# Optimization experiments

Hardware: AMD Instinct MI355X
Metric: run time of the kernel (lower is better)

Reference implementation:

```python
import jax, jax.numpy as jnp
import numpy as np

B, S, D, H, DFF = 2, 2048, 1024, 16, 4096
DK = D // H
EPS = 1e-6


def setup_inputs() -> dict:
    key = jax.random.key(0)
    ks = jax.random.split(key, 16)
    sd = 0.02
    inp = {
        "x": jax.random.normal(ks[0], (B, S, D), jnp.float32),
        "mask": jnp.zeros((1, 1, S, S), jnp.float32),
        "wq": jax.random.normal(ks[1], (D, D), jnp.float32) * sd,
        "bq": jnp.zeros((D,), jnp.float32),
        "wk": jax.random.normal(ks[2], (D, D), jnp.float32) * sd,
        "bk": jnp.zeros((D,), jnp.float32),
        "wv": jax.random.normal(ks[3], (D, D), jnp.float32) * sd,
        "bv": jnp.zeros((D,), jnp.float32),
        "wo": jax.random.normal(ks[4], (D, D), jnp.float32) * sd,
        "bo": jnp.zeros((D,), jnp.float32),
        "w1": jax.random.normal(ks[5], (DFF, D), jnp.float32) * sd,
        "b1": jnp.zeros((DFF,), jnp.float32),
        "w2": jax.random.normal(ks[6], (D, DFF), jnp.float32) * sd,
        "b2": jnp.zeros((D,), jnp.float32),
        "alpha": jnp.ones((1,), jnp.float32),
        "gamma": jnp.zeros((1,), jnp.float32),
    }
    return inp


def _layer_norm(x, alpha, gamma):
    mean = jnp.mean(x, axis=-1, keepdims=True)
    var = jnp.mean((x - mean) ** 2, axis=-1, keepdims=True)
    return alpha * (x - mean) / jnp.sqrt(var + EPS) + gamma


def reference(x, mask, wq, bq, wk, bk, wv, bv, wo, bo, w1, b1, w2, b2, alpha, gamma):
    # --- multi-head attention (hand-rolled, full NxN scores) ---
    q = (x @ wq.T + bq).reshape(B, S, H, DK).transpose(0, 2, 1, 3)  # [B,H,S,DK]
    k = (x @ wk.T + bk).reshape(B, S, H, DK).transpose(0, 2, 1, 3)
    v = (x @ wv.T + bv).reshape(B, S, H, DK).transpose(0, 2, 1, 3)
    scores = jnp.einsum('bhqd,bhkd->bhqk', q, k) / np.sqrt(DK)  # [B,H,S,S]
    scores = scores + mask
    attn = jax.nn.softmax(scores, axis=-1)
    ctx = jnp.einsum('bhqk,bhkd->bhqd', attn, v)  # [B,H,S,DK]
    ctx = ctx.transpose(0, 2, 1, 3).reshape(B, S, D)
    attn_out = ctx @ wo.T + bo
    # residual + LayerNorm (dropout is identity in eval)
    out1 = _layer_norm(x + attn_out, alpha, gamma)
    # --- position-wise feed-forward ---
    ffn = jax.nn.relu(out1 @ w1.T + b1) @ w2.T + b2
    out2 = _layer_norm(out1 + ffn, alpha, gamma)
    return out2
```

## Files before the change

### kernel.cpp

```cpp
#include <hip/hip_runtime.h>


typedef float  f32x4   __attribute__((ext_vector_type(4)));
typedef float  f32x16  __attribute__((ext_vector_type(16)));
typedef __bf16 bf16x8  __attribute__((ext_vector_type(8)));
typedef __bf16 bf16x4  __attribute__((ext_vector_type(4)));

#define DEVI static __device__ __forceinline__

DEVI f32x4 mfma16(bf16x8 a, bf16x8 b, f32x4 c) {
    return __builtin_amdgcn_mfma_f32_16x16x32_bf16(a, b, c, 0, 0, 0);
}
DEVI f32x16 mfma32(bf16x8 a, bf16x8 b, f32x16 c) {
    return __builtin_amdgcn_mfma_f32_32x32x16_bf16(a, b, c, 0, 0, 0);
}

DEVI void gll16(const void* g, void* l) {
    __builtin_amdgcn_global_load_lds(
        (__attribute__((address_space(1))) void*)g,
        (__attribute__((address_space(3))) void*)l, 16, 0, 0);
}

DEVI __bf16 f2bf(float f) { return (__bf16)f; }

DEVI unsigned cvtpk_bf16(float a, float b) {
    unsigned d;
    asm("v_cvt_pk_bf16_f32 %0, %1, %2" : "=v"(d) : "v"(a), "v"(b));
    return d;
}
DEVI void permswap(unsigned& a, unsigned& b) {
    asm("v_permlane32_swap_b32 %0, %1" : "+v"(a), "+v"(b));
}
DEVI void permswapf(float& a, float& b) {
    asm("v_permlane32_swap_b32 %0, %1" : "+v"(a), "+v"(b));
}

__global__ void init_flag_kernel(int* f) { *f = 0; }

__global__ void mask_scan_kernel(const float* __restrict__ m, int* __restrict__ flag) {
    size_t i = (size_t)blockIdx.x * 256 + threadIdx.x;
    const float4* p = (const float4*)m;
    float4 a = p[i * 2], b = p[i * 2 + 1];
    bool nz = a.x != 0.f || a.y != 0.f || a.z != 0.f || a.w != 0.f ||
              b.x != 0.f || b.y != 0.f || b.z != 0.f || b.w != 0.f;
    if (__ballot(nz)) { if ((threadIdx.x & 63) == 0) atomicOr(flag, 1); }
}

__global__ void cast_bf16_kernel(const float* __restrict__ in, __bf16* __restrict__ out, int n8) {
    int i = blockIdx.x * 256 + threadIdx.x;
    if (i >= n8) return;
    const float4* p = (const float4*)in + (size_t)i * 2;
    float4 a = p[0], b = p[1];
    bf16x8 o = { (__bf16)a.x, (__bf16)a.y, (__bf16)a.z, (__bf16)a.w,
                 (__bf16)b.x, (__bf16)b.y, (__bf16)b.z, (__bf16)b.w };
    *(bf16x8*)(out + (size_t)i * 8) = o;
}

__global__ __launch_bounds__(256) void cast_weights_kernel(
    const float* __restrict__ wq, const float* __restrict__ wk,
    const float* __restrict__ wv, const float* __restrict__ wo,
    const float* __restrict__ w1, const float* __restrict__ w2,
    __bf16* __restrict__ wqb, __bf16* __restrict__ wkb,
    __bf16* __restrict__ wvb, __bf16* __restrict__ wob,
    __bf16* __restrict__ w1b, __bf16* __restrict__ w2b) {
    int i = blockIdx.x * 256 + threadIdx.x;
    const float* src; __bf16* dst; int off;
    if      (i <  131072) { src = wq; dst = wqb; off = i; }
    else if (i <  262144) { src = wk; dst = wkb; off = i -  131072; }
    else if (i <  393216) { src = wv; dst = wvb; off = i -  262144; }
    else if (i <  524288) { src = wo; dst = wob; off = i -  393216; }
    else if (i < 1048576) { src = w1; dst = w1b; off = i -  524288; }
    else                  { src = w2; dst = w2b; off = i - 1048576; }
    const float4* p = (const float4*)src + (size_t)off * 2;
    float4 a = p[0], b = p[1];
    bf16x8 o = { (__bf16)a.x, (__bf16)a.y, (__bf16)a.z, (__bf16)a.w,
                 (__bf16)b.x, (__bf16)b.y, (__bf16)b.z, (__bf16)b.w };
    *(bf16x8*)(dst + (size_t)off * 8) = o;
}

__global__ __launch_bounds__(256) void add_ln_kernel(
    const float* __restrict__ X, const float* __restrict__ Y,
    const float* __restrict__ alphap, const float* __restrict__ gammap,
    float* __restrict__ outF, __bf16* __restrict__ outB) {
    const int tid = threadIdx.x, lane = tid & 63, wid = tid >> 6;
    const size_t base = (size_t)blockIdx.x * 1024 + tid * 4;
    float4 xv = *(const float4*)&X[base];
    float4 yv = *(const float4*)&Y[base];
    float vx = xv.x + yv.x, vy = xv.y + yv.y, vz = xv.z + yv.z, vw = xv.w + yv.w;
    float s = vx + vy + vz + vw;
    #pragma unroll
    for (int o = 32; o; o >>= 1) s += __shfl_xor(s, o);
    __shared__ float red[4];
    if (lane == 0) red[wid] = s;
    __syncthreads();
    float mean = (red[0] + red[1] + red[2] + red[3]) * (1.0f / 1024.0f);
    float dx = vx - mean, dy = vy - mean, dz = vz - mean, dw = vw - mean;
    float s2 = dx * dx + dy * dy + dz * dz + dw * dw;
    #pragma unroll
    for (int o = 32; o; o >>= 1) s2 += __shfl_xor(s2, o);
    __syncthreads();
    if (lane == 0) red[wid] = s2;
    __syncthreads();
    float var = (red[0] + red[1] + red[2] + red[3]) * (1.0f / 1024.0f);
    float rstd = rsqrtf(var + 1e-6f);
    float a = alphap[0], g = gammap[0];
    float4 o4 = { a * dx * rstd + g, a * dy * rstd + g, a * dz * rstd + g, a * dw * rstd + g };
    *(float4*)&outF[base] = o4;
    if (outB) {
        bf16x4 ob = { f2bf(o4.x), f2bf(o4.y), f2bf(o4.z), f2bf(o4.w) };
        *(bf16x4*)&outB[base] = ob;
    }
}

template <int N, int K, int BN, int MODE>
__global__ __launch_bounds__(256, 3) void gemm_bt_kernel(
    const __bf16* __restrict__ A, const __bf16* __restrict__ W,
    const float* __restrict__ bias, void* __restrict__ outp) {
    constexpr int WN = BN / 2;
    constexpr int NI = WN / 16;
    __shared__ __bf16 lsA[128 * 64];
    __shared__ __bf16 lsB[BN * 64];
    const int tid = threadIdx.x, wid = tid >> 6, lane = tid & 63;
    const int wr = wid >> 1, wc = wid & 1, l15 = lane & 15, hi = lane >> 4;
    const int m0 = blockIdx.y * 128, n0 = blockIdx.x * BN;
    f32x4 acc[4][NI] = {};
    for (int kt = 0; kt < K / 64; ++kt) {
        #pragma unroll
        for (int i = 0; i < 4; ++i) {
            int row = wid * 32 + i * 8 + (lane >> 3);
            gll16(A + (size_t)(m0 + row) * K + kt * 64 + ((lane & 7) ^ (row & 7)) * 8,
                  &lsA[(wid * 32 + i * 8) * 64]);
        }
        #pragma unroll
        for (int i = 0; i < BN / 32; ++i) {
            int row = wid * (BN / 4) + i * 8 + (lane >> 3);
            gll16(W + (size_t)(n0 + row) * K + kt * 64 + ((lane & 7) ^ (row & 7)) * 8,
                  &lsB[(wid * (BN / 4) + i * 8) * 64]);
        }
        __syncthreads();
        #pragma unroll
        for (int s = 0; s < 2; ++s) {
            bf16x8 af[4], bfv[NI];
            #pragma unroll
            for (int mi = 0; mi < 4; ++mi) {
                int row = wr * 64 + mi * 16 + l15;
                af[mi] = *(const bf16x8*)&lsA[row * 64 + (((s * 4 + hi) ^ (row & 7)) * 8)];
            }
            #pragma unroll
            for (int ni = 0; ni < NI; ++ni) {
                int row = wc * WN + ni * 16 + l15;
                bfv[ni] = *(const bf16x8*)&lsB[row * 64 + (((s * 4 + hi) ^ (row & 7)) * 8)];
            }
            #pragma unroll
            for (int mi = 0; mi < 4; ++mi)
                #pragma unroll
                for (int ni = 0; ni < NI; ++ni)
                    acc[mi][ni] = mfma16(af[mi], bfv[ni], acc[mi][ni]);
        }
        __syncthreads();
    }
    #pragma unroll
    for (int ni = 0; ni < NI; ++ni) {
        int col = n0 + wc * WN + ni * 16 + l15;
        float bv = bias[col];
        #pragma unroll
        for (int mi = 0; mi < 4; ++mi) {
            int rowb = m0 + wr * 64 + mi * 16 + hi * 4;
            #pragma unroll
            for (int r = 0; r < 4; ++r) {
                float v = acc[mi][ni][r] + bv;
                if (MODE == 0) {
                    ((float*)outp)[(size_t)(rowb + r) * N + col] = v;
                } else {
                    v = fmaxf(v, 0.f);
                    ((__bf16*)outp)[(size_t)(rowb + r) * N + col] = f2bf(v);
                }
            }
        }
    }
}

template <int N, int K>
__global__ __launch_bounds__(512, 1) void gemm_pipe_kernel(
    const __bf16* __restrict__ A, const __bf16* __restrict__ W,
    const float* __restrict__ bias, __bf16* __restrict__ outp) {
    constexpr int NT = K / 64;
    __shared__ __bf16 lsA[3][256 * 64];
    __shared__ __bf16 lsB[3][128 * 64];
    const int tid = threadIdx.x, wid = tid >> 6, lane = tid & 63;
    const int wr = wid >> 1, wc = wid & 1, l15 = lane & 15, hi = lane >> 4;
    const int bid = blockIdx.x;
    const int tile = (bid & 7) * 64 + (bid >> 3);
    const int m0 = (tile >> 5) * 256, n0 = (tile & 31) * 128;

    f32x4 acc[4][4] = {};

    const int rl = wid * 8 + (lane >> 3);
    const int c8 = lane & 7;

    auto stageT = [&](int slot, int kt) {
        #pragma unroll
        for (int j = 0; j < 4; ++j) {
            int r = j * 64 + rl;
            gll16(A + (size_t)(m0 + r) * K + kt * 64 + (c8 ^ (r & 7)) * 8,
                  &lsA[slot][(j * 64 + wid * 8) * 64]);
        }
        #pragma unroll
        for (int j = 0; j < 2; ++j) {
            int r = j * 64 + rl;
            gll16(W + (size_t)(n0 + r) * K + kt * 64 + (c8 ^ (r & 7)) * 8,
                  &lsB[slot][(j * 64 + wid * 8) * 64]);
        }
    };

    stageT(0, 0);
    stageT(1, 1);
    asm volatile("s_waitcnt vmcnt(6)\ns_barrier" ::: "memory");

    for (int t = 0; t < NT; ++t) {
        if (t + 2 < NT) stageT((t + 2) % 3, t + 2);
        const __bf16* As = &lsA[t % 3][0];
        const __bf16* Bs = &lsB[t % 3][0];
        __builtin_amdgcn_s_setprio(1);
        #pragma unroll
        for (int s = 0; s < 2; ++s) {
            bf16x8 af[4], bfv[4];
            #pragma unroll
            for (int mi = 0; mi < 4; ++mi) {
                int row = wr * 64 + mi * 16 + l15;
                af[mi] = *(const bf16x8*)&As[row * 64 + (((s * 4 + hi) ^ (row & 7)) * 8)];
            }
            #pragma unroll
            for (int ni = 0; ni < 4; ++ni) {
                int row = wc * 64 + ni * 16 + l15;
                bfv[ni] = *(const bf16x8*)&Bs[row * 64 + (((s * 4 + hi) ^ (row & 7)) * 8)];
            }
            #pragma unroll
            for (int mi = 0; mi < 4; ++mi)
                #pragma unroll
                for (int ni = 0; ni < 4; ++ni)
                    acc[mi][ni] = mfma16(af[mi], bfv[ni], acc[mi][ni]);
        }
        __builtin_amdgcn_s_setprio(0);
        if (t < NT - 2) {
            asm volatile("s_waitcnt vmcnt(6)\ns_barrier" ::: "memory");
        } else if (t == NT - 2) {
            asm volatile("s_waitcnt vmcnt(0)\ns_barrier" ::: "memory");
        }
    }

    #pragma unroll
    for (int ni = 0; ni < 4; ++ni) {
        int col = n0 + wc * 64 + ni * 16 + l15;
        float bv = bias[col];
        #pragma unroll
        for (int mi = 0; mi < 4; ++mi) {
            int rowb = m0 + wr * 64 + mi * 16 + hi * 4;
            #pragma unroll
            for (int r = 0; r < 4; ++r) {
                float v = fmaxf(acc[mi][ni][r] + bv, 0.f);
                outp[(size_t)(rowb + r) * N + col] = f2bf(v);
            }
        }
    }
}

__global__ __launch_bounds__(256, 3) void gemm_qkv_kernel(
    const __bf16* __restrict__ A,
    const __bf16* __restrict__ wq, const __bf16* __restrict__ wk, const __bf16* __restrict__ wv,
    const float* __restrict__ bq, const float* __restrict__ bk, const float* __restrict__ bv,
    __bf16* __restrict__ q, __bf16* __restrict__ k, __bf16* __restrict__ vt) {
    constexpr int K = 1024;
    const int z = blockIdx.z;
    const __bf16* W = (z == 0) ? wq : (z == 1) ? wk : wv;
    const float* bias = (z == 0) ? bq : (z == 1) ? bk : bv;
    __shared__ __bf16 lsA[128 * 64];
    __shared__ __bf16 lsB[128 * 64];
    const int tid = threadIdx.x, wid = tid >> 6, lane = tid & 63;
    const int wr = wid >> 1, wc = wid & 1, l15 = lane & 15, hi = lane >> 4;
    const int m0 = blockIdx.y * 128, n0 = blockIdx.x * 128;
    f32x4 acc[4][4] = {};
    for (int kt = 0; kt < K / 64; ++kt) {
        #pragma unroll
        for (int i = 0; i < 4; ++i) {
            int row = wid * 32 + i * 8 + (lane >> 3);
            gll16(A + (size_t)(m0 + row) * K + kt * 64 + ((lane & 7) ^ (row & 7)) * 8,
                  &lsA[(wid * 32 + i * 8) * 64]);
            gll16(W + (size_t)(n0 + row) * K + kt * 64 + ((lane & 7) ^ (row & 7)) * 8,
                  &lsB[(wid * 32 + i * 8) * 64]);
        }
        __syncthreads();
        #pragma unroll
        for (int s = 0; s < 2; ++s) {
            bf16x8 af[4], bfv[4];
            #pragma unroll
            for (int mi = 0; mi < 4; ++mi) {
                int row = wr * 64 + mi * 16 + l15;
                af[mi] = *(const bf16x8*)&lsA[row * 64 + (((s * 4 + hi) ^ (row & 7)) * 8)];
            }
            #pragma unroll
            for (int ni = 0; ni < 4; ++ni) {
                int row = wc * 64 + ni * 16 + l15;
                bfv[ni] = *(const bf16x8*)&lsB[row * 64 + (((s * 4 + hi) ^ (row & 7)) * 8)];
            }
            #pragma unroll
            for (int mi = 0; mi < 4; ++mi)
                #pragma unroll
                for (int ni = 0; ni < 4; ++ni)
                    acc[mi][ni] = mfma16(af[mi], bfv[ni], acc[mi][ni]);
        }
        __syncthreads();
    }
    const float scale = (z == 0) ? 0.125f * 1.4426950408889634f : 1.0f;
    #pragma unroll
    for (int ni = 0; ni < 4; ++ni) {
        int col = n0 + wc * 64 + ni * 16 + l15;
        int h = col >> 6, dk = col & 63;
        float bvv = bias[col];
        #pragma unroll
        for (int mi = 0; mi < 4; ++mi) {
            int rowb = m0 + wr * 64 + mi * 16 + hi * 4;
            int b_ = rowb >> 11, sb = rowb & 2047;
            if (z < 2) {
                __bf16* dst = (z == 0) ? q : k;
                #pragma unroll
                for (int r = 0; r < 4; ++r)
                    dst[((size_t)(b_ * 16 + h) * 2048 + sb + r) * 64 + dk] =
                        f2bf((acc[mi][ni][r] + bvv) * scale);
            } else {
                bf16x4 o = { f2bf(acc[mi][ni][0] + bvv), f2bf(acc[mi][ni][1] + bvv),
                             f2bf(acc[mi][ni][2] + bvv), f2bf(acc[mi][ni][3] + bvv) };
                *(bf16x4*)&vt[((size_t)(b_ * 16 + h) * 64 + dk) * 2048 + sb] = o;
            }
        }
    }
}

__global__ __launch_bounds__(256, 2) void flash_attn_kernel(
    const __bf16* __restrict__ Q, const __bf16* __restrict__ Kx,
    const __bf16* __restrict__ VT, const float* __restrict__ mask,
    const int* __restrict__ mflag, __bf16* __restrict__ ctx) {
    __shared__ __bf16 Kl[2][64 * 64];
    __shared__ __bf16 Vl[2][64 * 64];
    const int lane = threadIdx.x & 63, wid = threadIdx.x >> 6;
    const int l31 = lane & 31, h = lane >> 5;
    const int id = blockIdx.x;
    const int xcd = id & 7, rest = id >> 3;
    const int qt = rest & 15;
    const int bh = (rest >> 4) * 8 + xcd;
    const int q0 = qt * 128 + wid * 32;

    bf16x8 qf[4];
    const size_t qrow = (size_t)bh * 2048 + q0 + l31;
    #pragma unroll
    for (int st = 0; st < 4; ++st)
        qf[st] = *(const bf16x8*)&Q[qrow * 64 + st * 16 + h * 8];

    const __bf16* kbase = Kx + (size_t)bh * 2048 * 64;
    const __bf16* vbase = VT + (size_t)bh * 64 * 2048;

    f32x16 c0 = {}, c1 = {};
    f32x16 lv = {};
    const bool useMask = (*mflag != 0);

    const int r0 = wid * 16;
    const int rA = r0 + (lane >> 3);
    const int rB = rA + 8;
    const int cA = (lane & 7) ^ (rA & 7);
    const int cB = (lane & 7) ^ (rB & 7);

    auto stage = [&](int b, int t) {
        gll16(kbase + (size_t)(t * 64 + rA) * 64 + cA * 8, &Kl[b][r0 * 64]);
        gll16(kbase + (size_t)(t * 64 + rB) * 64 + cB * 8, &Kl[b][(r0 + 8) * 64]);
        gll16(vbase + (size_t)rA * 2048 + t * 64 + cA * 8, &Vl[b][r0 * 64]);
        gll16(vbase + (size_t)rB * 2048 + t * 64 + cB * 8, &Vl[b][(r0 + 8) * 64]);
    };

    stage(0, 0);
    __syncthreads();
    int cur = 0;

    for (int t = 0; t < 32; ++t) {
        const int tn = (t + 1 < 32) ? t + 1 : t;
        stage(cur ^ 1, tn);
        #pragma unroll
        for (int s = 0; s < 2; ++s) {
            const int krow = s * 32 + l31;
            f32x16 sc = {};
            __builtin_amdgcn_s_setprio(1);
            #pragma unroll
            for (int st = 0; st < 4; ++st) {
                bf16x8 kf = *(const bf16x8*)&Kl[cur][krow * 64 + (((st * 2 + h) ^ (krow & 7)) * 8)];
                sc = mfma32(kf, qf[st], sc);
            }
            __builtin_amdgcn_s_setprio(0);
            if (useMask) {
                #pragma unroll
                for (int r = 0; r < 16; ++r) {
                    int kv = t * 64 + s * 32 + (r & 3) + 8 * (r >> 2) + 4 * h;
                    sc[r] += mask[(size_t)(q0 + l31) * 2048 + kv] * 1.4426950408889634f;
                }
            }
            #pragma unroll
            for (int r = 0; r < 16; ++r) sc[r] = exp2f(sc[r] - 40.0f);
            lv += sc;
            unsigned w0 = cvtpk_bf16(sc[0], sc[1]),   w2 = cvtpk_bf16(sc[4], sc[5]);
            unsigned w1 = cvtpk_bf16(sc[2], sc[3]),   w3 = cvtpk_bf16(sc[6], sc[7]);
            permswap(w0, w2); permswap(w1, w3);
            unsigned w4 = cvtpk_bf16(sc[8], sc[9]),   w6 = cvtpk_bf16(sc[12], sc[13]);
            unsigned w5 = cvtpk_bf16(sc[10], sc[11]), w7 = cvtpk_bf16(sc[14], sc[15]);
            permswap(w4, w6); permswap(w5, w7);
            uint4 u0 = { w0, w1, w2, w3 }, u1 = { w4, w5, w6, w7 };
            bf16x8 pb0, pb1;
            __builtin_memcpy(&pb0, &u0, 16);
            __builtin_memcpy(&pb1, &u1, 16);
            const int vr0 = l31, vr1 = 32 + l31;
            bf16x8 v00 = *(const bf16x8*)&Vl[cur][vr0 * 64 + (((s * 4 + 0 + h) ^ (vr0 & 7)) * 8)];
            bf16x8 v01 = *(const bf16x8*)&Vl[cur][vr0 * 64 + (((s * 4 + 2 + h) ^ (vr0 & 7)) * 8)];
            bf16x8 v10 = *(const bf16x8*)&Vl[cur][vr1 * 64 + (((s * 4 + 0 + h) ^ (vr1 & 7)) * 8)];
            bf16x8 v11 = *(const bf16x8*)&Vl[cur][vr1 * 64 + (((s * 4 + 2 + h) ^ (vr1 & 7)) * 8)];
            __builtin_amdgcn_s_setprio(1);
            c0 = mfma32(v00, pb0, c0);
            c0 = mfma32(v01, pb1, c0);
            c1 = mfma32(v10, pb0, c1);
            c1 = mfma32(v11, pb1, c1);
            __builtin_amdgcn_s_setprio(0);
        }
        __syncthreads();
        cur ^= 1;
    }

    float y8[8], y4[4];
    #pragma unroll
    for (int r = 0; r < 8; ++r) y8[r] = lv[2 * r] + lv[2 * r + 1];
    #pragma unroll
    for (int r = 0; r < 4; ++r) y4[r] = y8[2 * r] + y8[2 * r + 1];
    float ls = (y4[0] + y4[1]) + (y4[2] + y4[3]);
    float la = ls, lb = ls;
    permswapf(la, lb);
    const float rinv = 1.0f / (la + lb);

    const int b_ = bh >> 4, h_ = bh & 15;
    const size_t obase = ((size_t)b_ * 2048 + q0 + l31) * 1024 + (size_t)h_ * 64;
    #pragma unroll
    for (int g = 0; g < 4; ++g) {
        bf16x4 o0 = { f2bf(c0[4 * g + 0] * rinv), f2bf(c0[4 * g + 1] * rinv),
                      f2bf(c0[4 * g + 2] * rinv), f2bf(c0[4 * g + 3] * rinv) };
        *(bf16x4*)&ctx[obase + g * 8 + h * 4] = o0;
        bf16x4 o1 = { f2bf(c1[4 * g + 0] * rinv), f2bf(c1[4 * g + 1] * rinv),
                      f2bf(c1[4 * g + 2] * rinv), f2bf(c1[4 * g + 3] * rinv) };
        *(bf16x4*)&ctx[obase + 32 + g * 8 + h * 4] = o1;
    }
}

extern "C" void kernel_launch(void* const* d_in, const int* in_sizes, int n_in,
                              void* d_out, int out_size, void* d_ws, size_t ws_size,
                              hipStream_t stream) {
    const float* x     = (const float*)d_in[0];
    const float* mask  = (const float*)d_in[1];
    const float* wq    = (const float*)d_in[2];
    const float* bq    = (const float*)d_in[3];
    const float* wk    = (const float*)d_in[4];
    const float* bk    = (const float*)d_in[5];
    const float* wv    = (const float*)d_in[6];
    const float* bv    = (const float*)d_in[7];
    const float* wo    = (const float*)d_in[8];
    const float* bo    = (const float*)d_in[9];
    const float* w1    = (const float*)d_in[10];
    const float* b1    = (const float*)d_in[11];
    const float* w2    = (const float*)d_in[12];
    const float* b2    = (const float*)d_in[13];
    const float* alpha = (const float*)d_in[14];
    const float* gamma = (const float*)d_in[15];

    char* ws = (char*)d_ws;
    const size_t MB = 1u << 20;
    __bf16* xb    = (__bf16*)(ws + 0 * MB);
    __bf16* qb    = (__bf16*)(ws + 8 * MB);
    __bf16* kb    = (__bf16*)(ws + 16 * MB);
    __bf16* vtb   = (__bf16*)(ws + 24 * MB);
    __bf16* ctxb  = (__bf16*)(ws + 32 * MB);
    __bf16* wqb   = (__bf16*)(ws + 40 * MB);
    __bf16* wkb   = (__bf16*)(ws + 42 * MB);
    __bf16* wvb   = (__bf16*)(ws + 44 * MB);
    __bf16* wob   = (__bf16*)(ws + 46 * MB);
    __bf16* w1b   = (__bf16*)(ws + 48 * MB);
    __bf16* w2b   = (__bf16*)(ws + 56 * MB);
    float*  attn  = (float*)(ws + 64 * MB);
    float*  out1  = (float*)(ws + 80 * MB);
    __bf16* out1b = (__bf16*)(ws + 96 * MB);
    __bf16* hid   = (__bf16*)(ws + 104 * MB);
    int*    mflag = (int*)(ws + 136 * MB);
    if (ws_size < 136 * MB + 64) return;

    init_flag_kernel<<<1, 1, 0, stream>>>(mflag);
    mask_scan_kernel<<<2048, 256, 0, stream>>>(mask, mflag);

    cast_bf16_kernel<<<2048, 256, 0, stream>>>(x, xb, 524288);
    cast_weights_kernel<<<6144, 256, 0, stream>>>(wq, wk, wv, wo, w1, w2,
                                                  wqb, wkb, wvb, wob, w1b, w2b);

    gemm_qkv_kernel<<<dim3(8, 32, 3), 256, 0, stream>>>(xb, wqb, wkb, wvb, bq, bk, bv,
                                                        qb, kb, vtb);
    flash_attn_kernel<<<dim3(512), 256, 0, stream>>>(qb, kb, vtb, mask, mflag, ctxb);
    gemm_bt_kernel<1024, 1024, 64, 0><<<dim3(16, 32), 256, 0, stream>>>(ctxb, wob, bo, attn);
    add_ln_kernel<<<4096, 256, 0, stream>>>(x, attn, alpha, gamma, out1, out1b);
    gemm_pipe_kernel<4096, 1024><<<dim3(512), 512, 0, stream>>>(out1b, w1b, b1, hid);
    gemm_bt_kernel<1024, 4096, 64, 0><<<dim3(16, 32), 256, 0, stream>>>(hid, w2b, b2, attn);
    add_ln_kernel<<<4096, 256, 0, stream>>>(out1, attn, alpha, gamma, (float*)d_out, nullptr);
}
```

Before: 273.3 us.

## Merge cast kernels, store intermediates in bf16, replace FFN1 GEMM with 128x128 tiles

Merges the x and weight bf16 casts into a single launch. Stores the attention-projection and FFN-down outputs as bf16 instead of fp32, and drops the fp32 out1 copy, so the second LayerNorm reads the bf16 residual. This cuts intermediate memory traffic at some precision cost in the residual path. It also replaces the 512-thread 256x128 pipelined FFN1 GEMM with a 256-thread 128x128 tile kernel using K=32 triple buffering, running 3 blocks per CU and more blocks overall.

```diff
diff --git a/kernel.cpp b/kernel.cpp
--- a/kernel.cpp
+++ b/kernel.cpp
@@ -46,31 +46,24 @@
     if (__ballot(nz)) { if ((threadIdx.x & 63) == 0) atomicOr(flag, 1); }
 }
 
-__global__ void cast_bf16_kernel(const float* __restrict__ in, __bf16* __restrict__ out, int n8) {
-    int i = blockIdx.x * 256 + threadIdx.x;
-    if (i >= n8) return;
-    const float4* p = (const float4*)in + (size_t)i * 2;
-    float4 a = p[0], b = p[1];
-    bf16x8 o = { (__bf16)a.x, (__bf16)a.y, (__bf16)a.z, (__bf16)a.w,
-                 (__bf16)b.x, (__bf16)b.y, (__bf16)b.z, (__bf16)b.w };
-    *(bf16x8*)(out + (size_t)i * 8) = o;
-}
-
-__global__ __launch_bounds__(256) void cast_weights_kernel(
+__global__ __launch_bounds__(256) void cast_all_kernel(
+    const float* __restrict__ x,
     const float* __restrict__ wq, const float* __restrict__ wk,
     const float* __restrict__ wv, const float* __restrict__ wo,
     const float* __restrict__ w1, const float* __restrict__ w2,
+    __bf16* __restrict__ xb,
     __bf16* __restrict__ wqb, __bf16* __restrict__ wkb,
     __bf16* __restrict__ wvb, __bf16* __restrict__ wob,
     __bf16* __restrict__ w1b, __bf16* __restrict__ w2b) {
     int i = blockIdx.x * 256 + threadIdx.x;
     const float* src; __bf16* dst; int off;
-    if      (i <  131072) { src = wq; dst = wqb; off = i; }
-    else if (i <  262144) { src = wk; dst = wkb; off = i -  131072; }
-    else if (i <  393216) { src = wv; dst = wvb; off = i -  262144; }
-    else if (i <  524288) { src = wo; dst = wob; off = i -  393216; }
-    else if (i < 1048576) { src = w1; dst = w1b; off = i -  524288; }
-    else                  { src = w2; dst = w2b; off = i - 1048576; }
+    if      (i <  524288) { src = x;  dst = xb;  off = i; }
+    else if (i <  655360) { src = wq; dst = wqb; off = i -  524288; }
+    else if (i <  786432) { src = wk; dst = wkb; off = i -  655360; }
+    else if (i <  917504) { src = wv; dst = wvb; off = i -  786432; }
+    else if (i < 1048576) { src = wo; dst = wob; off = i -  917504; }
+    else if (i < 1572864) { src = w1; dst = w1b; off = i - 1048576; }
+    else                  { src = w2; dst = w2b; off = i - 1572864; }
     const float4* p = (const float4*)src + (size_t)off * 2;
     float4 a = p[0], b = p[1];
     bf16x8 o = { (__bf16)a.x, (__bf16)a.y, (__bf16)a.z, (__bf16)a.w,
@@ -78,14 +71,26 @@
     *(bf16x8*)(dst + (size_t)off * 8) = o;
 }
 
+template <int XBF, int YBF>
 __global__ __launch_bounds__(256) void add_ln_kernel(
-    const float* __restrict__ X, const float* __restrict__ Y,
+    const void* __restrict__ Xv, const void* __restrict__ Yv,
     const float* __restrict__ alphap, const float* __restrict__ gammap,
     float* __restrict__ outF, __bf16* __restrict__ outB) {
     const int tid = threadIdx.x, lane = tid & 63, wid = tid >> 6;
     const size_t base = (size_t)blockIdx.x * 1024 + tid * 4;
-    float4 xv = *(const float4*)&X[base];
-    float4 yv = *(const float4*)&Y[base];
+    float4 xv, yv;
+    if (XBF) {
+        bf16x4 t = *(const bf16x4*)((const __bf16*)Xv + base);
+        xv.x = (float)t[0]; xv.y = (float)t[1]; xv.z = (float)t[2]; xv.w = (float)t[3];
+    } else {
+        xv = *(const float4*)((const float*)Xv + base);
+    }
+    if (YBF) {
+        bf16x4 t = *(const bf16x4*)((const __bf16*)Yv + base);
+        yv.x = (float)t[0]; yv.y = (float)t[1]; yv.z = (float)t[2]; yv.w = (float)t[3];
+    } else {
+        yv = *(const float4*)((const float*)Yv + base);
+    }
     float vx = xv.x + yv.x, vy = xv.y + yv.y, vz = xv.z + yv.z, vw = xv.w + yv.w;
     float s = vx + vy + vz + vw;
     #pragma unroll
@@ -105,7 +110,7 @@
     float rstd = rsqrtf(var + 1e-6f);
     float a = alphap[0], g = gammap[0];
     float4 o4 = { a * dx * rstd + g, a * dy * rstd + g, a * dz * rstd + g, a * dw * rstd + g };
-    *(float4*)&outF[base] = o4;
+    if (outF) *(float4*)&outF[base] = o4;
     if (outB) {
         bf16x4 ob = { f2bf(o4.x), f2bf(o4.y), f2bf(o4.z), f2bf(o4.w) };
         *(bf16x4*)&outB[base] = ob;
@@ -171,9 +176,11 @@
                 float v = acc[mi][ni][r] + bv;
                 if (MODE == 0) {
                     ((float*)outp)[(size_t)(rowb + r) * N + col] = v;
-                } else {
+                } else if (MODE == 1) {
                     v = fmaxf(v, 0.f);
                     ((__bf16*)outp)[(size_t)(rowb + r) * N + col] = f2bf(v);
+                } else {
+                    ((__bf16*)outp)[(size_t)(rowb + r) * N + col] = f2bf(v);
                 }
             }
         }
@@ -181,69 +188,58 @@
 }
 
 template <int N, int K>
-__global__ __launch_bounds__(512, 1) void gemm_pipe_kernel(
+__global__ __launch_bounds__(256, 3) void gemm_t3_kernel(
     const __bf16* __restrict__ A, const __bf16* __restrict__ W,
     const float* __restrict__ bias, __bf16* __restrict__ outp) {
-    constexpr int NT = K / 64;
-    __shared__ __bf16 lsA[3][256 * 64];
-    __shared__ __bf16 lsB[3][128 * 64];
+    constexpr int NT = K / 32;
+    __shared__ __bf16 lsA[3][128 * 32];
+    __shared__ __bf16 lsB[3][128 * 32];
     const int tid = threadIdx.x, wid = tid >> 6, lane = tid & 63;
     const int wr = wid >> 1, wc = wid & 1, l15 = lane & 15, hi = lane >> 4;
-    const int bid = blockIdx.x;
-    const int tile = (bid & 7) * 64 + (bid >> 3);
-    const int m0 = (tile >> 5) * 256, n0 = (tile & 31) * 128;
+    const int m0 = blockIdx.y * 128, n0 = blockIdx.x * 128;
 
     f32x4 acc[4][4] = {};
 
-    const int rl = wid * 8 + (lane >> 3);
-    const int c8 = lane & 7;
-
-    auto stageT = [&](int slot, int kt) {
-        #pragma unroll
-        for (int j = 0; j < 4; ++j) {
-            int r = j * 64 + rl;
-            gll16(A + (size_t)(m0 + r) * K + kt * 64 + (c8 ^ (r & 7)) * 8,
-                  &lsA[slot][(j * 64 + wid * 8) * 64]);
-        }
-        #pragma unroll
-        for (int j = 0; j < 2; ++j) {
-            int r = j * 64 + rl;
-            gll16(W + (size_t)(n0 + r) * K + kt * 64 + (c8 ^ (r & 7)) * 8,
-                  &lsB[slot][(j * 64 + wid * 8) * 64]);
-        }
+    const int srow0 = wid * 32 + (lane >> 2);
+    const int srow1 = srow0 + 16;
+    const int sc0 = (lane & 3) ^ (srow0 & 3);
+    const int sc1 = (lane & 3) ^ (srow1 & 3);
+
+    auto stage = [&](int slot, int kt) {
+        gll16(A + (size_t)(m0 + srow0) * K + kt * 32 + sc0 * 8, &lsA[slot][(wid * 32) * 32]);
+        gll16(A + (size_t)(m0 + srow1) * K + kt * 32 + sc1 * 8, &lsA[slot][(wid * 32 + 16) * 32]);
+        gll16(W + (size_t)(n0 + srow0) * K + kt * 32 + sc0 * 8, &lsB[slot][(wid * 32) * 32]);
+        gll16(W + (size_t)(n0 + srow1) * K + kt * 32 + sc1 * 8, &lsB[slot][(wid * 32 + 16) * 32]);
     };
 
-    stageT(0, 0);
-    stageT(1, 1);
-    asm volatile("s_waitcnt vmcnt(6)\ns_barrier" ::: "memory");
+    stage(0, 0);
+    stage(1, 1);
+    asm volatile("s_waitcnt vmcnt(4)\ns_barrier" ::: "memory");
 
     for (int t = 0; t < NT; ++t) {
-        if (t + 2 < NT) stageT((t + 2) % 3, t + 2);
+        if (t + 2 < NT) stage((t + 2) % 3, t + 2);
         const __bf16* As = &lsA[t % 3][0];
         const __bf16* Bs = &lsB[t % 3][0];
+        bf16x8 af[4], bfv[4];
+        #pragma unroll
+        for (int mi = 0; mi < 4; ++mi) {
+            int row = wr * 64 + mi * 16 + l15;
+            af[mi] = *(const bf16x8*)&As[row * 32 + ((hi ^ (row & 3)) * 8)];
+        }
+        #pragma unroll
+        for (int ni = 0; ni < 4; ++ni) {
+            int row = wc * 64 + ni * 16 + l15;
+            bfv[ni] = *(const bf16x8*)&Bs[row * 32 + ((hi ^ (row & 3)) * 8)];
+        }
         __builtin_amdgcn_s_setprio(1);
         #pragma unroll
-        for (int s = 0; s < 2; ++s) {
-            bf16x8 af[4], bfv[4];
-            #pragma unroll
-            for (int mi = 0; mi < 4; ++mi) {
-                int row = wr * 64 + mi * 16 + l15;
-                af[mi] = *(const bf16x8*)&As[row * 64 + (((s * 4 + hi) ^ (row & 7)) * 8)];
-            }
-            #pragma unroll
-            for (int ni = 0; ni < 4; ++ni) {
-                int row = wc * 64 + ni * 16 + l15;
-                bfv[ni] = *(const bf16x8*)&Bs[row * 64 + (((s * 4 + hi) ^ (row & 7)) * 8)];
-            }
-            #pragma unroll
-            for (int mi = 0; mi < 4; ++mi)
-                #pragma unroll
-                for (int ni = 0; ni < 4; ++ni)
-                    acc[mi][ni] = mfma16(af[mi], bfv[ni], acc[mi][ni]);
-        }
+        for (int mi = 0; mi < 4; ++mi)
+            #pragma unroll
+            for (int ni = 0; ni < 4; ++ni)
+                acc[mi][ni] = mfma16(af[mi], bfv[ni], acc[mi][ni]);
         __builtin_amdgcn_s_setprio(0);
         if (t < NT - 2) {
-            asm volatile("s_waitcnt vmcnt(6)\ns_barrier" ::: "memory");
+            asm volatile("s_waitcnt vmcnt(4)\ns_barrier" ::: "memory");
         } else if (t == NT - 2) {
             asm volatile("s_waitcnt vmcnt(0)\ns_barrier" ::: "memory");
         }
@@ -486,8 +482,7 @@
     __bf16* wob   = (__bf16*)(ws + 46 * MB);
     __bf16* w1b   = (__bf16*)(ws + 48 * MB);
     __bf16* w2b   = (__bf16*)(ws + 56 * MB);
-    float*  attn  = (float*)(ws + 64 * MB);
-    float*  out1  = (float*)(ws + 80 * MB);
+    __bf16* attnb = (__bf16*)(ws + 64 * MB);
     __bf16* out1b = (__bf16*)(ws + 96 * MB);
     __bf16* hid   = (__bf16*)(ws + 104 * MB);
     int*    mflag = (int*)(ws + 136 * MB);
@@ -496,16 +491,15 @@
     init_flag_kernel<<<1, 1, 0, stream>>>(mflag);
     mask_scan_kernel<<<2048, 256, 0, stream>>>(mask, mflag);
 
-    cast_bf16_kernel<<<2048, 256, 0, stream>>>(x, xb, 524288);
-    cast_weights_kernel<<<6144, 256, 0, stream>>>(wq, wk, wv, wo, w1, w2,
-                                                  wqb, wkb, wvb, wob, w1b, w2b);
+    cast_all_kernel<<<8192, 256, 0, stream>>>(x, wq, wk, wv, wo, w1, w2,
+                                              xb, wqb, wkb, wvb, wob, w1b, w2b);
 
     gemm_qkv_kernel<<<dim3(8, 32, 3), 256, 0, stream>>>(xb, wqb, wkb, wvb, bq, bk, bv,
                                                         qb, kb, vtb);
     flash_attn_kernel<<<dim3(512), 256, 0, stream>>>(qb, kb, vtb, mask, mflag, ctxb);
-    gemm_bt_kernel<1024, 1024, 64, 0><<<dim3(16, 32), 256, 0, stream>>>(ctxb, wob, bo, attn);
-    add_ln_kernel<<<4096, 256, 0, stream>>>(x, attn, alpha, gamma, out1, out1b);
-    gemm_pipe_kernel<4096, 1024><<<dim3(512), 512, 0, stream>>>(out1b, w1b, b1, hid);
-    gemm_bt_kernel<1024, 4096, 64, 0><<<dim3(16, 32), 256, 0, stream>>>(hid, w2b, b2, attn);
-    add_ln_kernel<<<4096, 256, 0, stream>>>(out1, attn, alpha, gamma, (float*)d_out, nullptr);
-}
+    gemm_bt_kernel<1024, 1024, 64, 2><<<dim3(16, 32), 256, 0, stream>>>(ctxb, wob, bo, attnb);
+    add_ln_kernel<0, 1><<<4096, 256, 0, stream>>>(x, attnb, alpha, gamma, nullptr, out1b);
+    gemm_t3_kernel<4096, 1024><<<dim3(32, 32), 256, 0, stream>>>(out1b, w1b, b1, hid);
+    gemm_bt_kernel<1024, 4096, 64, 2><<<dim3(16, 32), 256, 0, stream>>>(hid, w2b, b2, attnb);
+    add_ln_kernel<1, 1><<<4096, 256, 0, stream>>>(out1b, attnb, alpha, gamma, (float*)d_out, nullptr);
+}
```

Result: faster. 266.0 us (-2.7%).
